# Kernel optimization log

Hardware: AMD Instinct MI355X
Metric: run time of the kernel (lower is better)

## Reference

```python
import jax, jax.numpy as jnp
import numpy as np

NUM_HEADS = 12


def setup_inputs() -> dict:
    key = jax.random.key(0)
    ks = jax.random.split(key, 8)
    B, D, H, W, C = 4, 8, 14, 14, 768
    hd = C // NUM_HEADS
    return {
        "x": jax.random.normal(ks[0], (B, D, H, W, C), jnp.float32),
        "qkv_w": jax.random.normal(ks[1], (C, 3 * C), jnp.float32) * (C ** -0.5),
        "qkv_b": jax.random.normal(ks[2], (3 * C,), jnp.float32) * 0.02,
        "proj_w": jax.random.normal(ks[3], (C, C), jnp.float32) * (C ** -0.5),
        "proj_b": jax.random.normal(ks[4], (C,), jnp.float32) * 0.02,
        "rel_pos_d": jax.random.normal(ks[5], (2 * D - 1, hd), jnp.float32) * 0.02,
        "rel_pos_h": jax.random.normal(ks[6], (2 * H - 1, hd), jnp.float32) * 0.02,
        "rel_pos_w": jax.random.normal(ks[7], (2 * W - 1, hd), jnp.float32) * 0.02,
    }


def _rel_table(table, n):
    # q_size == k_size == n; relative coords in [0, 2n-2]
    idx = jnp.arange(n)[:, None] - jnp.arange(n)[None, :] + (n - 1)
    return table[idx]  # [n, n, head_dim]


def reference(x, qkv_w, qkv_b, proj_w, proj_b, rel_pos_d, rel_pos_h, rel_pos_w):
    B, D, H, W, C = x.shape
    hd = C // NUM_HEADS
    scale = hd ** -0.5
    N = D * H * W
    BH = B * NUM_HEADS

    qkv = x @ qkv_w + qkv_b  # [B,D,H,W,3C]
    qkv = qkv.reshape(B, N, 3, NUM_HEADS, hd).transpose(2, 0, 3, 1, 4).reshape(3, BH, N, hd)
    q, k, v = qkv[0], qkv[1], qkv[2]

    attn = jnp.einsum('bnc,bmc->bnm', q * scale, k)  # [BH, N, N]

    # decomposed 3D relative position bias
    Rd = _rel_table(rel_pos_d, D)  # [D,D,hd]
    Rh = _rel_table(rel_pos_h, H)  # [H,H,hd]
    Rw = _rel_table(rel_pos_w, W)  # [W,W,hd]
    r_q = q.reshape(BH, D, H, W, hd)
    rel_d = jnp.einsum('bdhwc,dkc->bdhwk', r_q, Rd)  # [BH,D,H,W,D]
    rel_h = jnp.einsum('bdhwc,hkc->bdhwk', r_q, Rh)  # [BH,D,H,W,H]
    rel_w = jnp.einsum('bdhwc,wkc->bdhwk', r_q, Rw)  # [BH,D,H,W,W]
    attn = (attn.reshape(BH, D, H, W, D, H, W)
            + rel_d[:, :, :, :, :, None, None]
            + rel_h[:, :, :, :, None, :, None]
            + rel_w[:, :, :, :, None, None, :]).reshape(BH, N, N)

    attn = jax.nn.softmax(attn, axis=-1)
    out = jnp.einsum('bnm,bmc->bnc', attn, v)  # [BH,N,hd]
    out = out.reshape(B, NUM_HEADS, D, H, W, hd).transpose(0, 2, 3, 4, 1, 5).reshape(B, D, H, W, C)
    return out @ proj_w + proj_b
```

## Files before the change

### kernel.cpp

```cpp
#include <hip/hip_runtime.h>


typedef __bf16 bf16x8 __attribute__((ext_vector_type(8)));
typedef float f32x4 __attribute__((ext_vector_type(4)));

#define MFMA16(a, b, c) __builtin_amdgcn_mfma_f32_16x16x32_bf16((a), (b), (c), 0, 0, 0)

#if __has_builtin(__builtin_amdgcn_exp2f)
#define EXP2(x) __builtin_amdgcn_exp2f(x)
#else
#define EXP2(x) exp2f(x)
#endif

static __device__ __forceinline__ unsigned short f2bf(float f) {
    union { float f; unsigned int u; } v; v.f = f;
    unsigned int u = v.u;
    return (unsigned short)((u + 0x7fffu + ((u >> 16) & 1u)) >> 16);
}

static __device__ __forceinline__ bf16x8 ld_bf8(const unsigned short* p) {
    return *reinterpret_cast<const bf16x8*>(p);
}

static __device__ __forceinline__ void dma16(const void* g, void* l) {
    __builtin_amdgcn_global_load_lds(
        (const __attribute__((address_space(1))) void*)g,
        (__attribute__((address_space(3))) void*)l, 16, 0, 0);
}


__global__ void k_cvt_x(const float* __restrict__ x, unsigned short* __restrict__ xbf, int n4) {
    int i = blockIdx.x * blockDim.x + threadIdx.x;
    if (i < n4) {
        float4 v = reinterpret_cast<const float4*>(x)[i];
        ushort4 o;
        o.x = f2bf(v.x); o.y = f2bf(v.y); o.z = f2bf(v.z); o.w = f2bf(v.w);
        reinterpret_cast<ushort4*>(xbf)[i] = o;
    }
}

__global__ __launch_bounds__(256) void k_transpose(const float* __restrict__ w,
                                                   unsigned short* __restrict__ wt,
                                                   int K, int N) {
    __shared__ float tile[64][65];
    int kt = blockIdx.x * 64;
    int nt = blockIdx.y * 64;
    int tid = threadIdx.x;
    int r = tid >> 2;
    int cg = tid & 3;
#pragma unroll
    for (int i = 0; i < 4; ++i) {
        int c = cg * 16 + i * 4;
        float4 v = *reinterpret_cast<const float4*>(&w[(size_t)(kt + r) * N + nt + c]);
        tile[r][c + 0] = v.x; tile[r][c + 1] = v.y; tile[r][c + 2] = v.z; tile[r][c + 3] = v.w;
    }
    __syncthreads();
#pragma unroll
    for (int i = 0; i < 4; ++i) {
        int c = cg * 16 + i * 4;
        ushort4 o;
        o.x = f2bf(tile[c + 0][r]);
        o.y = f2bf(tile[c + 1][r]);
        o.z = f2bf(tile[c + 2][r]);
        o.w = f2bf(tile[c + 3][r]);
        *reinterpret_cast<ushort4*>(&wt[(size_t)(nt + r) * K + kt + c]) = o;
    }
}

__global__ void k_tables(const float* __restrict__ rd, const float* __restrict__ rh,
                         const float* __restrict__ rw, unsigned short* __restrict__ T) {
    int i = blockIdx.x * blockDim.x + threadIdx.x;
    if (i < 80 * 64) {
        int row = i >> 6, c = i & 63;
        float v = 0.f;
        if (row < 15) v = rd[row * 64 + c];
        else if (row < 42) v = rh[(row - 15) * 64 + c];
        else if (row < 69) v = rw[(row - 42) * 64 + c];
        T[i] = f2bf(v * 1.44269504f);
    }
}

__global__ void k_fill_ind(unsigned short* __restrict__ indb) {
    int i = blockIdx.x * blockDim.x + threadIdx.x;
    if (i < 1600 * 64) {
        int key = i >> 6, c = i & 63;
        unsigned short v = 0;
        if (key < 1568) {
            int kd = key / 196;
            int r = key - kd * 196;
            int kh = r / 14;
            int kw = r - kh * 14;
            if (c == kd || c == 8 + kh || c == 22 + kw) v = 0x3F80;
        } else {
            if (c == 36) v = 0x3F80;
        }
        indb[i] = v;
    }
}

static __device__ __forceinline__ void gemm_core(const unsigned short* __restrict__ A,
                                                 const unsigned short* __restrict__ B,
                                                 int M_base, int N_base,
                                                 char* smem, f32x4 acc[4][4]) {
    const int lane = threadIdx.x & 63;
    const int wid = threadIdx.x >> 6;
    const int ww = wid & 1, wh = wid >> 1;
    const int quad = lane >> 4, l16 = lane & 15;
    const int sr = lane >> 3, sc = lane & 7;
    unsigned short* sA = (unsigned short*)smem;
    unsigned short* sB = (unsigned short*)(smem + 16384);

    for (int kt = 0; kt < 12; ++kt) {
#pragma unroll
        for (int j = 0; j < 4; ++j) {
            int loc = wid * 32 + j * 8 + sr;
            int gc = ((sc + loc) & 7) * 16;
            dma16((const char*)A + (size_t)(M_base + loc) * 1536 + kt * 128 + gc,
                  (char*)sA + (wid * 32 + j * 8) * 128);
            dma16((const char*)B + (size_t)(N_base + loc) * 1536 + kt * 128 + gc,
                  (char*)sB + (wid * 32 + j * 8) * 128);
        }
        __syncthreads();
#pragma unroll
        for (int s = 0; s < 2; ++s) {
            bf16x8 af[4], bfr[4];
#pragma unroll
            for (int i = 0; i < 4; ++i) {
                int ar = wh * 64 + i * 16 + l16;
                af[i] = ld_bf8(sA + ar * 64 + (((s * 4 + quad) - ar) & 7) * 8);
                int br = ww * 64 + i * 16 + l16;
                bfr[i] = ld_bf8(sB + br * 64 + (((s * 4 + quad) - br) & 7) * 8);
            }
#pragma unroll
            for (int i = 0; i < 4; ++i)
#pragma unroll
                for (int j2 = 0; j2 < 4; ++j2)
                    acc[i][j2] = MFMA16(af[i], bfr[j2], acc[i][j2]);
        }
        __syncthreads();
    }
}

__global__ __launch_bounds__(256, 4) void k_qkv(const unsigned short* __restrict__ xbf,
                                                const unsigned short* __restrict__ w1t,
                                                const float* __restrict__ qkv_b,
                                                unsigned short* __restrict__ qb,
                                                unsigned short* __restrict__ kb2,
                                                unsigned short* __restrict__ vb) {
    __shared__ __align__(16) char smem[32768];
    f32x4 acc[4][4] = {};
    gemm_core(xbf, w1t, blockIdx.x * 128, blockIdx.y * 128, smem, acc);

    const int lane = threadIdx.x & 63;
    const int wid = threadIdx.x >> 6;
    const int ww = wid & 1, wh = wid >> 1;
    const int quad = lane >> 4, l16 = lane & 15;
#pragma unroll
    for (int j = 0; j < 4; ++j) {
        int n = blockIdx.y * 128 + ww * 64 + j * 16 + l16;
        float bias = qkv_b[n];
        int which = n / 768;
        int rem = n - which * 768;
        int head = rem >> 6;
        int c = rem & 63;
#pragma unroll
        for (int i = 0; i < 4; ++i) {
#pragma unroll
            for (int r = 0; r < 4; ++r) {
                int m = blockIdx.x * 128 + wh * 64 + i * 16 + quad * 4 + r;
                float val = acc[i][j][r] + bias;
                int b_ = m / 1568;
                int nn = m - b_ * 1568;
                size_t idx = ((size_t)(b_ * 12 + head) * 1568 + nn) * 64 + c;
                if (which == 0)      qb[idx] = f2bf(val);
                else if (which == 1) kb2[(((size_t)(b_ * 12 + head)) * 1600 + nn) * 64 + c] = f2bf(val * 0.18033688f);
                else                 vb[idx] = f2bf(val);
            }
        }
    }
}

__global__ __launch_bounds__(256) void k_vt(const unsigned short* __restrict__ vb,
                                            unsigned short* __restrict__ vtb) {
    __shared__ unsigned short t[64][72];
    int bh = blockIdx.y;
    int n0 = blockIdx.x * 64;
    int tid = threadIdx.x;
    int r = tid >> 2, cg = (tid & 3) * 16;
    int n = n0 + r;
    if (n > 1567) n = 1567;
    const unsigned short* src = vb + ((size_t)bh * 1568 + n) * 64 + cg;
    *reinterpret_cast<uint4*>(&t[r][cg]) = *reinterpret_cast<const uint4*>(src);
    *reinterpret_cast<uint4*>(&t[r][cg + 8]) = *reinterpret_cast<const uint4*>(src + 8);
    __syncthreads();
    int c = tid >> 2, ng = (tid & 3) * 16;
    if (n0 + ng < 1568) {
        unsigned short buf[16];
#pragma unroll
        for (int i = 0; i < 16; ++i) buf[i] = t[ng + i][c];
        unsigned short* dst = vtb + ((size_t)bh * 64 + c) * 1600 + n0 + ng;
        *reinterpret_cast<uint4*>(dst) = *reinterpret_cast<uint4*>(&buf[0]);
        *reinterpret_cast<uint4*>(dst + 8) = *reinterpret_cast<uint4*>(&buf[8]);
    }
}

__global__ __launch_bounds__(256, 3) void k_attn(const unsigned short* __restrict__ qb,
                                                 const unsigned short* __restrict__ kb2,
                                                 const unsigned short* __restrict__ indb,
                                                 const unsigned short* __restrict__ vtb,
                                                 const unsigned short* __restrict__ Tbf,
                                                 unsigned short* __restrict__ obf) {
    __shared__ __align__(16) char smem[52224];
    const int lane = threadIdx.x & 63;
    const int wid = threadIdx.x >> 6;
    const int quad = lane >> 4;
    const int l16 = lane & 15;
    const int sr = lane >> 3;
    const int sc = lane & 7;
    const int bh = blockIdx.x;
    const int qt = blockIdx.y;

    unsigned short* pw = (unsigned short*)(smem + 43008 + wid * 2304);
    unsigned short* tR = (unsigned short*)(smem + wid * 5120);
    unsigned short* tB = (unsigned short*)(smem + 21504 + wid * 4608);

    const int iA = wid * 64 + lane;
    const int ioA = (iA / 5) * 128 + (iA % 5) * 16;
    const int iB = 256 + lane;
    const int ioB = (iB / 5) * 128 + (iB % 5) * 16;

    bf16x8 a_q0[2], a_q1[2], a_b0[2], a_b1[2];
#pragma unroll
    for (int mt = 0; mt < 2; ++mt) {
        int qrow = qt * 128 + wid * 32 + mt * 16 + l16;
        if (qrow > 1567) qrow = 1567;
        const unsigned short* qp = qb + ((size_t)bh * 1568 + qrow) * 64 + quad * 8;
        a_q0[mt] = ld_bf8(qp);
        a_q1[mt] = ld_bf8(qp + 32);
    }
#pragma unroll
    for (int mt = 0; mt < 2; ++mt) {
#pragma unroll
        for (int ng = 0; ng < 5; ++ng) {
            const unsigned short* tp = Tbf + (size_t)(ng * 16 + l16) * 64 + quad * 8;
            f32x4 t = {};
            t = MFMA16(a_q0[mt], ld_bf8(tp), t);
            t = MFMA16(a_q1[mt], ld_bf8(tp + 32), t);
#pragma unroll
            for (int r = 0; r < 4; ++r)
                tR[(mt * 16 + quad * 4 + r) * 80 + ng * 16 + l16] = f2bf(t[r]);
        }
    }
#pragma unroll
    for (int mt = 0; mt < 2; ++mt) {
        int gq = qt * 128 + wid * 32 + mt * 16 + l16;
        if (gq > 1567) gq = 1567;
        int qd = gq / 196;
        int rm = gq - qd * 196;
        int qh = rm / 14;
        int qw = rm - qh * 14;
        const unsigned short* qr = tR + (mt * 16 + l16) * 80;
        unsigned short* qxr = tB + (mt * 16 + l16) * 72;
#pragma unroll
        for (int t = 0; t < 16; ++t) {
            int dd = quad * 16 + t;
            unsigned short v = 0;
            if (dd < 8)        v = qr[qd - dd + 7];
            else if (dd < 22)  v = qr[15 + qh - (dd - 8) + 13];
            else if (dd < 36)  v = qr[42 + qw - (dd - 22) + 13];
            else if (dd == 36) v = 0xC6EA;
            qxr[dd] = v;
        }
    }
#pragma unroll
    for (int mt = 0; mt < 2; ++mt) {
        const unsigned short* qx = tB + (mt * 16 + l16) * 72;
        a_b0[mt] = ld_bf8(qx + quad * 8);
        a_b1[mt] = ld_bf8(qx + 32 + quad * 8);
    }
    __syncthreads();

    const char* kbh_b = (const char*)(kb2 + (size_t)bh * 1600 * 64);
    const char* ind_b = (const char*)indb;
    const char* vbh_b = (const char*)(vtb + (size_t)bh * 64 * 1600);

    auto stage = [&](char* sbase, int kb0) {
#pragma unroll
        for (int j = 0; j < 2; ++j) {
            int loc = wid * 16 + j * 8 + sr;
            int gc = ((sc + loc) & 7) * 16;
            dma16(kbh_b + (size_t)(kb0 + loc) * 128 + gc, sbase + (wid * 16 + j * 8) * 128);
            dma16(vbh_b + (size_t)loc * 3200 + (size_t)kb0 * 2 + gc,
                  sbase + 13312 + (wid * 16 + j * 8) * 128);
        }
        dma16(ind_b + (size_t)kb0 * 128 + ioA, sbase + 8192 + wid * 1024);
        if (wid == 0)
            dma16(ind_b + (size_t)kb0 * 128 + ioB, sbase + 8192 + 4096);
    };

    float l_p[2][4] = {};
    f32x4 Oacc[2][4] = {};

    stage(smem, 0);
    __syncthreads();

    for (int kt = 0; kt < 25; ++kt) {
        char* cur = smem + (kt & 1) * 21504;
        if (kt < 24) stage(smem + ((kt + 1) & 1) * 21504, (kt + 1) * 64);

        const unsigned short* sK = (const unsigned short*)cur;
        const unsigned short* sI = (const unsigned short*)(cur + 8192);
        const unsigned short* sV = (const unsigned short*)(cur + 13312);

        float p[2][4][4];
#pragma unroll
        for (int kg = 0; kg < 4; ++kg) {
            int key = kg * 16 + l16;
            const unsigned short* kr = sK + key * 64;
            bf16x8 bk0 = ld_bf8(kr + ((quad - key) & 7) * 8);
            bf16x8 bk1 = ld_bf8(kr + ((quad + 4 - key) & 7) * 8);
            const unsigned short* ir = sI + key * 40;
            bf16x8 bi0 = ld_bf8(ir + quad * 8);
            bf16x8 bi1 = ld_bf8(ir + 32 + quad * 8);
#pragma unroll
            for (int mt = 0; mt < 2; ++mt) {
                f32x4 t = {};
                t = MFMA16(a_q0[mt], bk0, t);
                t = MFMA16(a_q1[mt], bk1, t);
                t = MFMA16(a_b0[mt], bi0, t);
                t = MFMA16(a_b1[mt], bi1, t);
#pragma unroll
                for (int r = 0; r < 4; ++r) {
                    union { float f; unsigned int u; } c;
                    c.f = EXP2(t[r]);
                    c.u &= 0xFFFF0000u;
                    p[mt][kg][r] = c.f;
                    l_p[mt][r] += c.f;
                }
            }
        }
        bf16x8 v0[4], v1[4];
#pragma unroll
        for (int cg = 0; cg < 4; ++cg) {
            int dim = cg * 16 + l16;
            const unsigned short* vr = sV + dim * 64;
            v0[cg] = ld_bf8(vr + ((quad - dim) & 7) * 8);
            v1[cg] = ld_bf8(vr + ((quad + 4 - dim) & 7) * 8);
        }
#pragma unroll
        for (int mt = 0; mt < 2; ++mt) {
#pragma unroll
            for (int kg = 0; kg < 4; ++kg)
#pragma unroll
                for (int r = 0; r < 4; ++r) {
                    union { float f; unsigned int u; } c;
                    c.f = p[mt][kg][r];
                    pw[(quad * 4 + r) * 72 + kg * 16 + l16] = (unsigned short)(c.u >> 16);
                }
            const unsigned short* pr = pw + l16 * 72;
            bf16x8 ap0 = ld_bf8(pr + quad * 8);
            bf16x8 ap1 = ld_bf8(pr + 32 + quad * 8);
#pragma unroll
            for (int cg = 0; cg < 4; ++cg) {
                Oacc[mt][cg] = MFMA16(ap0, v0[cg], Oacc[mt][cg]);
                Oacc[mt][cg] = MFMA16(ap1, v1[cg], Oacc[mt][cg]);
            }
        }
        __syncthreads();
    }

    int b_ = bh / 12;
    int head = bh - b_ * 12;
    unsigned short* ob = obf + (size_t)b_ * 1568 * 768 + head * 64;
#pragma unroll
    for (int mt = 0; mt < 2; ++mt)
#pragma unroll
        for (int r = 0; r < 4; ++r) {
            float v = l_p[mt][r];
            v += __shfl_xor(v, 1);
            v += __shfl_xor(v, 2);
            v += __shfl_xor(v, 4);
            v += __shfl_xor(v, 8);
            int gq = qt * 128 + wid * 32 + mt * 16 + quad * 4 + r;
            if (gq < 1568) {
                float inv = 1.0f / v;
#pragma unroll
                for (int cg = 0; cg < 4; ++cg)
                    ob[(size_t)gq * 768 + cg * 16 + l16] = f2bf(Oacc[mt][cg][r] * inv);
            }
        }
}

__global__ __launch_bounds__(256, 3) void k_proj(const unsigned short* __restrict__ obf,
                                                 const unsigned short* __restrict__ w2t,
                                                 const float* __restrict__ proj_b,
                                                 float* __restrict__ out) {
    __shared__ __align__(16) char smem[32768];
    f32x4 acc[4][4] = {};
    gemm_core(obf, w2t, blockIdx.x * 128, blockIdx.y * 128, smem, acc);

    const int lane = threadIdx.x & 63;
    const int wid = threadIdx.x >> 6;
    const int ww = wid & 1, wh = wid >> 1;
    const int quad = lane >> 4, l16 = lane & 15;
#pragma unroll
    for (int j = 0; j < 4; ++j) {
        int n = blockIdx.y * 128 + ww * 64 + j * 16 + l16;
        float bias = proj_b[n];
#pragma unroll
        for (int i = 0; i < 4; ++i) {
#pragma unroll
            for (int r = 0; r < 4; ++r) {
                int m = blockIdx.x * 128 + wh * 64 + i * 16 + quad * 4 + r;
                out[(size_t)m * 768 + n] = acc[i][j][r] + bias;
            }
        }
    }
}

extern "C" void kernel_launch(void* const* d_in, const int* in_sizes, int n_in,
                              void* d_out, int out_size, void* d_ws, size_t ws_size,
                              hipStream_t stream) {
    const float* x      = (const float*)d_in[0];
    const float* qkv_w  = (const float*)d_in[1];
    const float* qkv_b  = (const float*)d_in[2];
    const float* proj_w = (const float*)d_in[3];
    const float* proj_b = (const float*)d_in[4];
    const float* rd     = (const float*)d_in[5];
    const float* rh     = (const float*)d_in[6];
    const float* rw     = (const float*)d_in[7];
    float* out = (float*)d_out;

    char* ws = (char*)d_ws;
    size_t off = 0;
    auto alloc = [&](size_t bytes) {
        char* p = ws + off;
        off += (bytes + 255) & ~(size_t)255;
        return p;
    };
    unsigned short* xbf  = (unsigned short*)alloc((size_t)6272 * 768 * 2);
    unsigned short* w1t  = (unsigned short*)alloc((size_t)2304 * 768 * 2);
    unsigned short* w2t  = (unsigned short*)alloc((size_t)768 * 768 * 2);
    unsigned short* Tbf  = (unsigned short*)alloc((size_t)80 * 64 * 2);
    unsigned short* qb   = (unsigned short*)alloc((size_t)48 * 1568 * 64 * 2);
    unsigned short* kb2  = (unsigned short*)alloc((size_t)48 * 1600 * 64 * 2);
    unsigned short* vtb  = (unsigned short*)alloc((size_t)48 * 64 * 1600 * 2);
    unsigned short* indb = (unsigned short*)alloc((size_t)1600 * 64 * 2);
    unsigned short* obf  = xbf;
    unsigned short* vb   = (unsigned short*)d_out;

    hipLaunchKernelGGL(k_cvt_x, dim3(4704), dim3(256), 0, stream, x, xbf, 1204224);
    hipLaunchKernelGGL(k_transpose, dim3(12, 36), dim3(256), 0, stream, qkv_w, w1t, 768, 2304);
    hipLaunchKernelGGL(k_transpose, dim3(12, 12), dim3(256), 0, stream, proj_w, w2t, 768, 768);
    hipLaunchKernelGGL(k_tables, dim3(20), dim3(256), 0, stream, rd, rh, rw, Tbf);
    hipLaunchKernelGGL(k_fill_ind, dim3(400), dim3(256), 0, stream, indb);
    hipLaunchKernelGGL(k_qkv, dim3(49, 18), dim3(256), 0, stream, xbf, w1t, qkv_b, qb, kb2, vb);
    hipLaunchKernelGGL(k_vt, dim3(25, 48), dim3(256), 0, stream, vb, vtb);
    hipLaunchKernelGGL(k_attn, dim3(48, 13), dim3(256), 0, stream, qb, kb2, indb, vtb, Tbf, obf);
    hipLaunchKernelGGL(k_proj, dim3(49, 6), dim3(256), 0, stream, obf, w2t, proj_b, out);
}
```

Baseline: 237.3 us.

## Merge preprocessing kernels into one launch and shrink projection GEMM M-tile

Five small preprocessing kernels (x conversion, two weight transposes, the bias tables, the indicator fill) are combined into one k_prep kernel that dispatches on block index. This removes four kernel launches and the gaps between them. Separately, the output projection GEMM switches to a 64x128 tile with a new gemm_core64. That doubles the grid from 294 to 588 blocks for better CU occupancy and raises the occupancy bound to 4, at the cost of less reuse of each B tile.

```diff
diff --git a/kernel.cpp b/kernel.cpp
--- a/kernel.cpp
+++ b/kernel.cpp
@@ -29,22 +29,12 @@
 }
 
 
-__global__ void k_cvt_x(const float* __restrict__ x, unsigned short* __restrict__ xbf, int n4) {
-    int i = blockIdx.x * blockDim.x + threadIdx.x;
-    if (i < n4) {
-        float4 v = reinterpret_cast<const float4*>(x)[i];
-        ushort4 o;
-        o.x = f2bf(v.x); o.y = f2bf(v.y); o.z = f2bf(v.z); o.w = f2bf(v.w);
-        reinterpret_cast<ushort4*>(xbf)[i] = o;
-    }
-}
-
-__global__ __launch_bounds__(256) void k_transpose(const float* __restrict__ w,
-                                                   unsigned short* __restrict__ wt,
-                                                   int K, int N) {
-    __shared__ float tile[64][65];
-    int kt = blockIdx.x * 64;
-    int nt = blockIdx.y * 64;
+static __device__ __forceinline__ void do_transpose(const float* __restrict__ w,
+                                                    unsigned short* __restrict__ wt,
+                                                    int K, int N, int bx, int by,
+                                                    float (*tile)[65]) {
+    int kt = bx * 64;
+    int nt = by * 64;
     int tid = threadIdx.x;
     int r = tid >> 2;
     int cg = tid & 3;
@@ -67,34 +57,59 @@
     }
 }
 
-__global__ void k_tables(const float* __restrict__ rd, const float* __restrict__ rh,
-                         const float* __restrict__ rw, unsigned short* __restrict__ T) {
-    int i = blockIdx.x * blockDim.x + threadIdx.x;
-    if (i < 80 * 64) {
-        int row = i >> 6, c = i & 63;
-        float v = 0.f;
-        if (row < 15) v = rd[row * 64 + c];
-        else if (row < 42) v = rh[(row - 15) * 64 + c];
-        else if (row < 69) v = rw[(row - 42) * 64 + c];
-        T[i] = f2bf(v * 1.44269504f);
-    }
-}
-
-__global__ void k_fill_ind(unsigned short* __restrict__ indb) {
-    int i = blockIdx.x * blockDim.x + threadIdx.x;
-    if (i < 1600 * 64) {
-        int key = i >> 6, c = i & 63;
-        unsigned short v = 0;
-        if (key < 1568) {
-            int kd = key / 196;
-            int r = key - kd * 196;
-            int kh = r / 14;
-            int kw = r - kh * 14;
-            if (c == kd || c == 8 + kh || c == 22 + kw) v = 0x3F80;
-        } else {
-            if (c == 36) v = 0x3F80;
-        }
-        indb[i] = v;
+__global__ __launch_bounds__(256) void k_prep(const float* __restrict__ x,
+                                              unsigned short* __restrict__ xbf,
+                                              const float* __restrict__ qkv_w,
+                                              unsigned short* __restrict__ w1t,
+                                              const float* __restrict__ proj_w,
+                                              unsigned short* __restrict__ w2t,
+                                              const float* __restrict__ rd,
+                                              const float* __restrict__ rh,
+                                              const float* __restrict__ rw,
+                                              unsigned short* __restrict__ Tbf,
+                                              unsigned short* __restrict__ indb) {
+    __shared__ float tile[64][65];
+    int bid = blockIdx.x;
+    if (bid < 4704) {
+        int i = bid * 256 + threadIdx.x;
+        if (i < 1204224) {
+            float4 v = reinterpret_cast<const float4*>(x)[i];
+            ushort4 o;
+            o.x = f2bf(v.x); o.y = f2bf(v.y); o.z = f2bf(v.z); o.w = f2bf(v.w);
+            reinterpret_cast<ushort4*>(xbf)[i] = o;
+        }
+    } else if (bid < 5136) {
+        int t = bid - 4704;
+        do_transpose(qkv_w, w1t, 768, 2304, t % 12, t / 12, tile);
+    } else if (bid < 5280) {
+        int t = bid - 5136;
+        do_transpose(proj_w, w2t, 768, 768, t % 12, t / 12, tile);
+    } else if (bid < 5300) {
+        int i = (bid - 5280) * 256 + threadIdx.x;
+        if (i < 80 * 64) {
+            int row = i >> 6, c = i & 63;
+            float v = 0.f;
+            if (row < 15) v = rd[row * 64 + c];
+            else if (row < 42) v = rh[(row - 15) * 64 + c];
+            else if (row < 69) v = rw[(row - 42) * 64 + c];
+            Tbf[i] = f2bf(v * 1.44269504f);
+        }
+    } else {
+        int i = (bid - 5300) * 256 + threadIdx.x;
+        if (i < 1600 * 64) {
+            int key = i >> 6, c = i & 63;
+            unsigned short v = 0;
+            if (key < 1568) {
+                int kd = key / 196;
+                int r = key - kd * 196;
+                int kh = r / 14;
+                int kw = r - kh * 14;
+                if (c == kd || c == 8 + kh || c == 22 + kw) v = 0x3F80;
+            } else {
+                if (c == 36) v = 0x3F80;
+            }
+            indb[i] = v;
+        }
     }
 }
 
@@ -136,6 +151,56 @@
 #pragma unroll
                 for (int j2 = 0; j2 < 4; ++j2)
                     acc[i][j2] = MFMA16(af[i], bfr[j2], acc[i][j2]);
+        }
+        __syncthreads();
+    }
+}
+
+static __device__ __forceinline__ void gemm_core64(const unsigned short* __restrict__ A,
+                                                   const unsigned short* __restrict__ B,
+                                                   int M_base, int N_base,
+                                                   char* smem, f32x4 acc[4][2]) {
+    const int lane = threadIdx.x & 63;
+    const int wid = threadIdx.x >> 6;
+    const int quad = lane >> 4, l16 = lane & 15;
+    const int sr = lane >> 3, sc = lane & 7;
+    unsigned short* sA = (unsigned short*)smem;
+    unsigned short* sB = (unsigned short*)(smem + 8192);
+
+    for (int kt = 0; kt < 12; ++kt) {
+#pragma unroll
+        for (int j = 0; j < 2; ++j) {
+            int loc = wid * 16 + j * 8 + sr;
+            int gc = ((sc + loc) & 7) * 16;
+            dma16((const char*)A + (size_t)(M_base + loc) * 1536 + kt * 128 + gc,
+                  (char*)sA + (wid * 16 + j * 8) * 128);
+        }
+#pragma unroll
+        for (int j = 0; j < 4; ++j) {
+            int loc = wid * 32 + j * 8 + sr;
+            int gc = ((sc + loc) & 7) * 16;
+            dma16((const char*)B + (size_t)(N_base + loc) * 1536 + kt * 128 + gc,
+                  (char*)sB + (wid * 32 + j * 8) * 128);
+        }
+        __syncthreads();
+#pragma unroll
+        for (int s = 0; s < 2; ++s) {
+            bf16x8 af[4], bfr[2];
+#pragma unroll
+            for (int i = 0; i < 4; ++i) {
+                int ar = i * 16 + l16;
+                af[i] = ld_bf8(sA + ar * 64 + (((s * 4 + quad) - ar) & 7) * 8);
+            }
+#pragma unroll
+            for (int j = 0; j < 2; ++j) {
+                int br = wid * 32 + j * 16 + l16;
+                bfr[j] = ld_bf8(sB + br * 64 + (((s * 4 + quad) - br) & 7) * 8);
+            }
+#pragma unroll
+            for (int i = 0; i < 4; ++i)
+#pragma unroll
+                for (int j = 0; j < 2; ++j)
+                    acc[i][j] = MFMA16(af[i], bfr[j], acc[i][j]);
         }
         __syncthreads();
     }
@@ -391,27 +456,26 @@
         }
 }
 
-__global__ __launch_bounds__(256, 3) void k_proj(const unsigned short* __restrict__ obf,
+__global__ __launch_bounds__(256, 4) void k_proj(const unsigned short* __restrict__ obf,
                                                  const unsigned short* __restrict__ w2t,
                                                  const float* __restrict__ proj_b,
                                                  float* __restrict__ out) {
-    __shared__ __align__(16) char smem[32768];
-    f32x4 acc[4][4] = {};
-    gemm_core(obf, w2t, blockIdx.x * 128, blockIdx.y * 128, smem, acc);
+    __shared__ __align__(16) char smem[24576];
+    f32x4 acc[4][2] = {};
+    gemm_core64(obf, w2t, blockIdx.x * 64, blockIdx.y * 128, smem, acc);
 
     const int lane = threadIdx.x & 63;
     const int wid = threadIdx.x >> 6;
-    const int ww = wid & 1, wh = wid >> 1;
     const int quad = lane >> 4, l16 = lane & 15;
 #pragma unroll
-    for (int j = 0; j < 4; ++j) {
-        int n = blockIdx.y * 128 + ww * 64 + j * 16 + l16;
+    for (int j = 0; j < 2; ++j) {
+        int n = blockIdx.y * 128 + wid * 32 + j * 16 + l16;
         float bias = proj_b[n];
 #pragma unroll
         for (int i = 0; i < 4; ++i) {
 #pragma unroll
             for (int r = 0; r < 4; ++r) {
-                int m = blockIdx.x * 128 + wh * 64 + i * 16 + quad * 4 + r;
+                int m = blockIdx.x * 64 + i * 16 + quad * 4 + r;
                 out[(size_t)m * 768 + n] = acc[i][j][r] + bias;
             }
         }
@@ -449,13 +513,10 @@
     unsigned short* obf  = xbf;
     unsigned short* vb   = (unsigned short*)d_out;
 
-    hipLaunchKernelGGL(k_cvt_x, dim3(4704), dim3(256), 0, stream, x, xbf, 1204224);
-    hipLaunchKernelGGL(k_transpose, dim3(12, 36), dim3(256), 0, stream, qkv_w, w1t, 768, 2304);
-    hipLaunchKernelGGL(k_transpose, dim3(12, 12), dim3(256), 0, stream, proj_w, w2t, 768, 768);
-    hipLaunchKernelGGL(k_tables, dim3(20), dim3(256), 0, stream, rd, rh, rw, Tbf);
-    hipLaunchKernelGGL(k_fill_ind, dim3(400), dim3(256), 0, stream, indb);
+    hipLaunchKernelGGL(k_prep, dim3(5700), dim3(256), 0, stream,
+                       x, xbf, qkv_w, w1t, proj_w, w2t, rd, rh, rw, Tbf, indb);
     hipLaunchKernelGGL(k_qkv, dim3(49, 18), dim3(256), 0, stream, xbf, w1t, qkv_b, qb, kb2, vb);
     hipLaunchKernelGGL(k_vt, dim3(25, 48), dim3(256), 0, stream, vb, vtb);
     hipLaunchKernelGGL(k_attn, dim3(48, 13), dim3(256), 0, stream, qb, kb2, indb, vtb, Tbf, obf);
-    hipLaunchKernelGGL(k_proj, dim3(49, 6), dim3(256), 0, stream, obf, w2t, proj_b, out);
-}
+    hipLaunchKernelGGL(k_proj, dim3(98, 6), dim3(256), 0, stream, obf, w2t, proj_b, out);
+}
```

New measurement: 226.6 us. 4.5% less time.
